# Kernel tuning notes

Hardware: AMD Instinct MI355X
Metric: run time of the kernel (lower is better)

The kernel has to match this reference:

```python
import jax, jax.numpy as jnp
import numpy as np

B, N_NODES, N_EDGES = 2, 40962, 327680
ND, ED, HD, L = 256, 64, 512, 16  # node_dim, edge_dim, hidden_dim, n_layers
LN_EPS = 1e-5


def _ln(x, g, b):
    m = jnp.mean(x, axis=-1, keepdims=True)
    v = jnp.var(x, axis=-1, keepdims=True)
    return (x - m) * jax.lax.rsqrt(v + LN_EPS) * g + b


def setup_inputs() -> dict:
    key = jax.random.key(0)
    ks = jax.random.split(key, 8)
    def w(k, shape, fan_in):
        return jax.random.normal(k, shape, jnp.float32) * (1.0 / np.sqrt(fan_in))
    node_features = jax.random.normal(ks[0], (B, N_NODES, ND), jnp.float32)
    edge_features = jax.random.normal(ks[1], (N_EDGES, ED), jnp.float32)
    edge_index = jax.random.randint(ks[2], (2, N_EDGES), 0, N_NODES, dtype=jnp.int32)
    ein, nin = ED + 2 * ND, ND + ED
    return {
        "node_features": node_features,
        "edge_features": edge_features,
        "We1": w(ks[3], (L, ein, HD), ein), "be1": jnp.zeros((L, HD), jnp.float32),
        "We2": w(ks[4], (L, HD, ED), HD),   "be2": jnp.zeros((L, ED), jnp.float32),
        "ge": jnp.ones((L, ED), jnp.float32), "ble": jnp.zeros((L, ED), jnp.float32),
        "Wn1": w(ks[5], (L, nin, HD), nin), "bn1": jnp.zeros((L, HD), jnp.float32),
        "Wn2": w(ks[6], (L, HD, ND), HD),   "bn2": jnp.zeros((L, ND), jnp.float32),
        "gn": jnp.ones((L, ND), jnp.float32), "bln": jnp.zeros((L, ND), jnp.float32),
        "edge_index": edge_index,
    }


def reference(node_features, edge_features, We1, be1, We2, be2, ge, ble,
              Wn1, bn1, Wn2, bn2, gn, bln, edge_index):
    src, dst = edge_index[0], edge_index[1]
    n = node_features.shape[-2]
    stacked = (We1, be1, We2, be2, ge, ble, Wn1, bn1, Wn2, bn2, gn, bln)

    def single(x0):  # x0: (N, ND) — original loops over batch; we vmap
        def layer(carry, p):
            x, e = carry
            we1, b1, we2, b2, g_e, b_e, wn1, nb1, wn2, nb2, g_n, b_n = p
            # edge update: gather endpoints, MLP, residual
            m = jnp.concatenate([e, x[src], x[dst]], axis=-1)   # (E, ED+2*ND)
            h = jax.nn.silu(m @ we1 + b1)                        # (E, HD)
            e = e + _ln(h @ we2 + b2, g_e, b_e)                  # (E, ED)
            # node update: scatter-sum messages to destinations, MLP, residual
            agg = jax.ops.segment_sum(e, dst, num_segments=n)    # (N, ED)
            h = jax.nn.silu(jnp.concatenate([x, agg], axis=-1) @ wn1 + nb1)
            x = x + _ln(h @ wn2 + nb2, g_n, b_n)                 # (N, ND)
            return (x, e), None
        (x, _e), _ = jax.lax.scan(layer, (x0, edge_features), stacked)
        return x

    return jax.vmap(single)(node_features)
```

## Files before the change

kernel.cpp:

```cpp
#include <hip/hip_runtime.h>
#include <hip/hip_bf16.h>

#define N_NODES 40962
#define N_EDGES 327680
#define NDIM 256
#define EDIM 64
#define HDIM 512
#define NLAYERS 16

using bf16_t = __bf16;
using bf16x4 = __bf16 __attribute__((ext_vector_type(4)));
using bf16x8 = __bf16 __attribute__((ext_vector_type(8)));
using f32x4  = float __attribute__((ext_vector_type(4)));

__device__ __forceinline__ void cvt_store4(bf16_t* p, float4 v) {
    bf16x4 t;
    t[0] = (bf16_t)v.x; t[1] = (bf16_t)v.y; t[2] = (bf16_t)v.z; t[3] = (bf16_t)v.w;
    *(bf16x4*)p = t;
}

__device__ __forceinline__ int clamp_idx(int v) {
    return v < 0 ? 0 : (v >= N_NODES ? N_NODES - 1 : v);
}

__global__ void repack_w(const float* __restrict__ src, bf16_t* __restrict__ dst,
                         int K, int N, int tilesPer) {
    int idx = blockIdx.x * 256 + threadIdx.x;
    int lane = idx & 63;
    int t = idx >> 6;
    int l = t / tilesPer;
    int tile = t % tilesPer;
    if (l >= NLAYERS) return;
    int ntN = N >> 4;
    int k0 = (tile / ntN) << 5;
    int n0 = (tile % ntN) << 4;
    int k = k0 + (lane >> 4) * 8;
    int n = n0 + (lane & 15);
    const float* s = src + (size_t)l * K * N + (size_t)k * N + n;
    bf16x8 v;
#pragma unroll
    for (int j = 0; j < 8; ++j) v[j] = (bf16_t)s[(size_t)j * N];
    *(bf16x8*)(dst + (size_t)idx * 8) = v;
}

__global__ void init_e2(const float* __restrict__ ef, bf16_t* __restrict__ es, int n8) {
    const size_t per = (size_t)N_EDGES * EDIM;
    for (int i = blockIdx.x * 256 + threadIdx.x; i < n8; i += gridDim.x * 256) {
        float4 a = *(const float4*)(ef + (size_t)i * 8);
        float4 b = *(const float4*)(ef + (size_t)i * 8 + 4);
        bf16x8 v;
        v[0] = (bf16_t)a.x; v[1] = (bf16_t)a.y; v[2] = (bf16_t)a.z; v[3] = (bf16_t)a.w;
        v[4] = (bf16_t)b.x; v[5] = (bf16_t)b.y; v[6] = (bf16_t)b.z; v[7] = (bf16_t)b.w;
        *(bf16x8*)(es + (size_t)i * 8) = v;
        *(bf16x8*)(es + per + (size_t)i * 8) = v;
    }
}

__global__ void zero_f32(float* __restrict__ p, int n4) {
    float4 z; z.x = z.y = z.z = z.w = 0.f;
    for (int i = blockIdx.x * 256 + threadIdx.x; i < n4; i += gridDim.x * 256)
        *(float4*)(p + (size_t)i * 4) = z;
}

__global__ __launch_bounds__(512, 4)
void edge_kernel(const float* __restrict__ xs, bf16_t* __restrict__ es,
                 float* __restrict__ agg, const int* __restrict__ eidx,
                 const bf16_t* __restrict__ w1p, const float* __restrict__ b1,
                 const bf16_t* __restrict__ w2p, const float* __restrict__ b2,
                 const float* __restrict__ gw, const float* __restrict__ bw) {
    __shared__ bf16_t smem[64 * 584];
    __shared__ int sSrc[64], sDst[64];
    float* red = (float*)(smem + 64 * 520);

    const int b   = blockIdx.y;
    const int e0  = blockIdx.x * 64;
    const int tid = threadIdx.x;

    const float* xb = xs + (size_t)b * N_NODES * NDIM;
    bf16_t* eb = es + (size_t)b * N_EDGES * EDIM;
    float* ab = agg + (size_t)b * N_NODES * EDIM;

    if (tid < 64) {
        sSrc[tid] = clamp_idx(eidx[e0 + tid]);
        sDst[tid] = clamp_idx(eidx[N_EDGES + e0 + tid]);
    }
    __syncthreads();

    {
        int r = tid >> 3, c = (tid & 7) << 3;
        *(bf16x8*)&smem[r * 584 + c] = *(const bf16x8*)(eb + (size_t)(e0 + r) * EDIM + c);
    }
#pragma unroll
    for (int k = 0; k < 8; ++k) {
        int i = tid + k * 512;
        int r = i >> 6, f = (i & 63) << 2;
        float4 v = *(const float4*)(xb + (size_t)sSrc[r] * NDIM + f);
        cvt_store4(&smem[r * 584 + 64 + f], v);
    }
#pragma unroll
    for (int k = 0; k < 8; ++k) {
        int i = tid + k * 512;
        int r = i >> 6, f = (i & 63) << 2;
        float4 v = *(const float4*)(xb + (size_t)sDst[r] * NDIM + f);
        cvt_store4(&smem[r * 584 + 320 + f], v);
    }
    __syncthreads();

    const int wv = tid >> 6, lane = tid & 63;
    const int m16 = lane & 15, quad = lane >> 4;

    float bias1[4];
#pragma unroll
    for (int nt = 0; nt < 4; ++nt) bias1[nt] = b1[wv * 64 + nt * 16 + m16];

    f32x4 acc1[4][4];
#pragma unroll
    for (int mt = 0; mt < 4; ++mt)
#pragma unroll
        for (int nt = 0; nt < 4; ++nt) acc1[mt][nt] = (f32x4){0.f, 0.f, 0.f, 0.f};

    const bf16x8* W1 = (const bf16x8*)w1p;
#pragma unroll 2
    for (int kc = 0; kc < 18; ++kc) {
        bf16x8 af[4];
#pragma unroll
        for (int mt = 0; mt < 4; ++mt)
            af[mt] = *(const bf16x8*)&smem[(mt * 16 + m16) * 584 + kc * 32 + quad * 8];
        bf16x8 bfr[4];
#pragma unroll
        for (int nt = 0; nt < 4; ++nt)
            bfr[nt] = W1[(size_t)(kc * 32 + wv * 4 + nt) * 64 + lane];
#pragma unroll
        for (int mt = 0; mt < 4; ++mt)
#pragma unroll
            for (int nt = 0; nt < 4; ++nt)
                acc1[mt][nt] = __builtin_amdgcn_mfma_f32_16x16x32_bf16(af[mt], bfr[nt], acc1[mt][nt], 0, 0, 0);
    }
    __syncthreads();

#pragma unroll
    for (int mt = 0; mt < 4; ++mt)
#pragma unroll
        for (int nt = 0; nt < 4; ++nt)
#pragma unroll
            for (int r = 0; r < 4; ++r) {
                int row = mt * 16 + quad * 4 + r;
                int col = wv * 64 + nt * 16 + m16;
                float v = acc1[mt][nt][r] + bias1[nt];
                v = v / (1.f + __expf(-v));
                smem[row * 520 + col] = (bf16_t)v;
            }
    __syncthreads();

    const int strip = wv >> 1, nh = wv & 1;
    f32x4 acc2[2];
#pragma unroll
    for (int nt = 0; nt < 2; ++nt) acc2[nt] = (f32x4){0.f, 0.f, 0.f, 0.f};
    const bf16x8* W2 = (const bf16x8*)w2p;
#pragma unroll 2
    for (int kc = 0; kc < 16; ++kc) {
        bf16x8 a2 = *(const bf16x8*)&smem[(strip * 16 + m16) * 520 + kc * 32 + quad * 8];
#pragma unroll
        for (int nt = 0; nt < 2; ++nt) {
            bf16x8 b2f = W2[(size_t)(kc * 4 + nh * 2 + nt) * 64 + lane];
            acc2[nt] = __builtin_amdgcn_mfma_f32_16x16x32_bf16(a2, b2f, acc2[nt], 0, 0, 0);
        }
    }

    float bias2[2], g2[2], bl2[2];
#pragma unroll
    for (int nt = 0; nt < 2; ++nt) {
        int c = nh * 32 + nt * 16 + m16;
        bias2[nt] = b2[c];
        g2[nt]    = gw[c];
        bl2[nt]   = bw[c];
    }
    float v[4][2];
#pragma unroll
    for (int r = 0; r < 4; ++r) {
        float s1 = 0.f, s2 = 0.f;
#pragma unroll
        for (int nt = 0; nt < 2; ++nt) {
            v[r][nt] = acc2[nt][r] + bias2[nt];
            s1 += v[r][nt]; s2 += v[r][nt] * v[r][nt];
        }
#pragma unroll
        for (int off = 1; off < 16; off <<= 1) {
            s1 += __shfl_xor(s1, off);
            s2 += __shfl_xor(s2, off);
        }
        if (m16 == 0) {
            int row = strip * 16 + quad * 4 + r;
            red[row * 4 + nh * 2 + 0] = s1;
            red[row * 4 + nh * 2 + 1] = s2;
        }
    }
    __syncthreads();

#pragma unroll
    for (int r = 0; r < 4; ++r) {
        int row = strip * 16 + quad * 4 + r;
        float s1 = red[row * 4 + 0] + red[row * 4 + 2];
        float s2 = red[row * 4 + 1] + red[row * 4 + 3];
        float mean = s1 * (1.f / 64.f);
        float var  = s2 * (1.f / 64.f) - mean * mean;
        float rstd = rsqrtf(fmaxf(var, 0.f) + 1e-5f);
        int eid = e0 + row;
        int d = sDst[row];
        bf16_t* ebr = eb + (size_t)eid * EDIM;
#pragma unroll
        for (int nt = 0; nt < 2; ++nt) {
            int c = nh * 32 + nt * 16 + m16;
            float ln = (v[r][nt] - mean) * rstd * g2[nt] + bl2[nt];
            float en = (float)ebr[c] + ln;
            ebr[c] = (bf16_t)en;
            atomicAdd(&ab[(size_t)d * EDIM + c], en);
        }
    }
}

__global__ __launch_bounds__(512, 4)
void node_kernel(float* __restrict__ xs, const float* __restrict__ agg,
                 const bf16_t* __restrict__ w1p, const float* __restrict__ b1,
                 const bf16_t* __restrict__ w2p, const float* __restrict__ b2,
                 const float* __restrict__ gw, const float* __restrict__ bw) {
    __shared__ bf16_t smem[64 * 528];
    float* red = (float*)(smem + 64 * 520);

    const int b   = blockIdx.y;
    const int n0  = blockIdx.x * 64;
    const int tid = threadIdx.x;

    float* xb = xs + (size_t)b * N_NODES * NDIM;
    const float* ab = agg + (size_t)b * N_NODES * EDIM;

    float4 z4; z4.x = z4.y = z4.z = z4.w = 0.f;
#pragma unroll
    for (int k = 0; k < 8; ++k) {
        int i = tid + k * 512;
        int r = i >> 6, f = (i & 63) << 2;
        int node = n0 + r;
        float4 v = (node < N_NODES) ? *(const float4*)(xb + (size_t)node * NDIM + f) : z4;
        cvt_store4(&smem[r * 328 + f], v);
    }
#pragma unroll
    for (int k = 0; k < 2; ++k) {
        int i = tid + k * 512;
        int r = i >> 4, f = (i & 15) << 2;
        int node = n0 + r;
        float4 v = (node < N_NODES) ? *(const float4*)(ab + (size_t)node * EDIM + f) : z4;
        cvt_store4(&smem[r * 328 + 256 + f], v);
    }
    __syncthreads();

    const int wv = tid >> 6, lane = tid & 63;
    const int m16 = lane & 15, quad = lane >> 4;

    float bias1[4];
#pragma unroll
    for (int nt = 0; nt < 4; ++nt) bias1[nt] = b1[wv * 64 + nt * 16 + m16];

    f32x4 acc1[4][4];
#pragma unroll
    for (int mt = 0; mt < 4; ++mt)
#pragma unroll
        for (int nt = 0; nt < 4; ++nt) acc1[mt][nt] = (f32x4){0.f, 0.f, 0.f, 0.f};

    const bf16x8* W1 = (const bf16x8*)w1p;
#pragma unroll 2
    for (int kc = 0; kc < 10; ++kc) {
        bf16x8 af[4];
#pragma unroll
        for (int mt = 0; mt < 4; ++mt)
            af[mt] = *(const bf16x8*)&smem[(mt * 16 + m16) * 328 + kc * 32 + quad * 8];
        bf16x8 bfr[4];
#pragma unroll
        for (int nt = 0; nt < 4; ++nt)
            bfr[nt] = W1[(size_t)(kc * 32 + wv * 4 + nt) * 64 + lane];
#pragma unroll
        for (int mt = 0; mt < 4; ++mt)
#pragma unroll
            for (int nt = 0; nt < 4; ++nt)
                acc1[mt][nt] = __builtin_amdgcn_mfma_f32_16x16x32_bf16(af[mt], bfr[nt], acc1[mt][nt], 0, 0, 0);
    }
    __syncthreads();

#pragma unroll
    for (int mt = 0; mt < 4; ++mt)
#pragma unroll
        for (int nt = 0; nt < 4; ++nt)
#pragma unroll
            for (int r = 0; r < 4; ++r) {
                int row = mt * 16 + quad * 4 + r;
                int col = wv * 64 + nt * 16 + m16;
                float v = acc1[mt][nt][r] + bias1[nt];
                v = v / (1.f + __expf(-v));
                smem[row * 520 + col] = (bf16_t)v;
            }
    __syncthreads();

    const int strip = wv >> 1, nh = wv & 1;
    f32x4 acc2[8];
#pragma unroll
    for (int nt = 0; nt < 8; ++nt) acc2[nt] = (f32x4){0.f, 0.f, 0.f, 0.f};
    const bf16x8* W2 = (const bf16x8*)w2p;
#pragma unroll 2
    for (int kc = 0; kc < 16; ++kc) {
        bf16x8 a2 = *(const bf16x8*)&smem[(strip * 16 + m16) * 520 + kc * 32 + quad * 8];
#pragma unroll
        for (int nt = 0; nt < 8; ++nt) {
            bf16x8 b2f = W2[(size_t)(kc * 16 + nh * 8 + nt) * 64 + lane];
            acc2[nt] = __builtin_amdgcn_mfma_f32_16x16x32_bf16(a2, b2f, acc2[nt], 0, 0, 0);
        }
    }

    float bias2[8], g8[8], bl8[8];
#pragma unroll
    for (int nt = 0; nt < 8; ++nt) {
        int c = nh * 128 + nt * 16 + m16;
        bias2[nt] = b2[c];
        g8[nt]    = gw[c];
        bl8[nt]   = bw[c];
    }
    float v[4][8];
#pragma unroll
    for (int r = 0; r < 4; ++r) {
        float s1 = 0.f, s2 = 0.f;
#pragma unroll
        for (int nt = 0; nt < 8; ++nt) {
            v[r][nt] = acc2[nt][r] + bias2[nt];
            s1 += v[r][nt]; s2 += v[r][nt] * v[r][nt];
        }
#pragma unroll
        for (int off = 1; off < 16; off <<= 1) {
            s1 += __shfl_xor(s1, off);
            s2 += __shfl_xor(s2, off);
        }
        if (m16 == 0) {
            int row = strip * 16 + quad * 4 + r;
            red[row * 4 + nh * 2 + 0] = s1;
            red[row * 4 + nh * 2 + 1] = s2;
        }
    }
    __syncthreads();

#pragma unroll
    for (int r = 0; r < 4; ++r) {
        int row = strip * 16 + quad * 4 + r;
        int node = n0 + row;
        if (node >= N_NODES) continue;
        float s1 = red[row * 4 + 0] + red[row * 4 + 2];
        float s2 = red[row * 4 + 1] + red[row * 4 + 3];
        float mean = s1 * (1.f / 256.f);
        float var  = s2 * (1.f / 256.f) - mean * mean;
        float rstd = rsqrtf(fmaxf(var, 0.f) + 1e-5f);
#pragma unroll
        for (int nt = 0; nt < 8; ++nt) {
            int c = nh * 128 + nt * 16 + m16;
            float ln = (v[r][nt] - mean) * rstd * g8[nt] + bl8[nt];
            xb[(size_t)node * NDIM + c] += ln;
        }
    }
}

extern "C" void kernel_launch(void* const* d_in, const int* in_sizes, int n_in,
                              void* d_out, int out_size, void* d_ws, size_t ws_size,
                              hipStream_t stream) {
    const float* nf   = (const float*)d_in[0];
    const float* ef   = (const float*)d_in[1];
    const float* We1  = (const float*)d_in[2];
    const float* be1  = (const float*)d_in[3];
    const float* We2  = (const float*)d_in[4];
    const float* be2  = (const float*)d_in[5];
    const float* ge   = (const float*)d_in[6];
    const float* ble  = (const float*)d_in[7];
    const float* Wn1  = (const float*)d_in[8];
    const float* bn1  = (const float*)d_in[9];
    const float* Wn2  = (const float*)d_in[10];
    const float* bn2  = (const float*)d_in[11];
    const float* gn   = (const float*)d_in[12];
    const float* bln  = (const float*)d_in[13];
    const int* eidx   = (const int*)d_in[14];

    float* xs = (float*)d_out;

    char* p = (char*)d_ws;
    bf16_t* es = (bf16_t*)p; p += (size_t)2 * N_EDGES * EDIM * 2;
    float*  ag = (float*)p;  p += (size_t)2 * N_NODES * EDIM * 4;
    bf16_t* w1ep = (bf16_t*)p; p += (size_t)NLAYERS * 576 * 512 * 2;
    bf16_t* w2ep = (bf16_t*)p; p += (size_t)NLAYERS * 512 * 64 * 2;
    bf16_t* w1np = (bf16_t*)p; p += (size_t)NLAYERS * 320 * 512 * 2;
    bf16_t* w2np = (bf16_t*)p; p += (size_t)NLAYERS * 512 * 256 * 2;

    repack_w<<<2304, 256, 0, stream>>>(We1, w1ep, 576, 512, 576);
    repack_w<<<256,  256, 0, stream>>>(We2, w2ep, 512, 64,  64);
    repack_w<<<1280, 256, 0, stream>>>(Wn1, w1np, 320, 512, 320);
    repack_w<<<1024, 256, 0, stream>>>(Wn2, w2np, 512, 256, 256);

    hipMemcpyAsync(xs, nf, (size_t)out_size * 4, hipMemcpyDeviceToDevice, stream);
    init_e2<<<2048, 256, 0, stream>>>(ef, es, N_EDGES * EDIM / 8);

    for (int l = 0; l < NLAYERS; ++l) {
        zero_f32<<<2048, 256, 0, stream>>>(ag, 2 * N_NODES * EDIM / 4);
        edge_kernel<<<dim3(N_EDGES / 64, 2), 512, 0, stream>>>(
            xs, es, ag, eidx,
            w1ep + (size_t)l * 576 * 512, be1 + l * 512,
            w2ep + (size_t)l * 512 * 64,  be2 + l * 64,
            ge + l * 64, ble + l * 64);
        node_kernel<<<dim3((N_NODES + 63) / 64, 2), 512, 0, stream>>>(
            xs, ag,
            w1np + (size_t)l * 320 * 512, bn1 + l * 512,
            w2np + (size_t)l * 512 * 256, bn2 + l * 256,
            gn + l * 256, bln + l * 256);
    }
}
```

Baseline: 13.29 ms.

## Replace atomic scatter with CSR gather aggregation and bf16 node mirror

Builds a destination-sorted CSR index once per call (histogram, scan, fill), and the node kernel now sums incoming edge features by gathering through it instead of the edge kernel doing fp32 atomicAdds into a zeroed buffer. It also keeps a bf16 copy of node features, updated in the node kernel, so the edge kernel gathers half as many bytes. Edge features are staged in shared memory and written back with vector stores. The cost is a serial single-block scan, per-node irregular gather loops with load imbalance, and aggregation summed from bf16-rounded edge values.

New measurement: 12.49 ms. 6.0% less time.

```diff
diff --git a/kernel.cpp b/kernel.cpp
--- a/kernel.cpp
+++ b/kernel.cpp
@@ -13,14 +13,15 @@
 using bf16x8 = __bf16 __attribute__((ext_vector_type(8)));
 using f32x4  = float __attribute__((ext_vector_type(4)));
 
-__device__ __forceinline__ void cvt_store4(bf16_t* p, float4 v) {
-    bf16x4 t;
-    t[0] = (bf16_t)v.x; t[1] = (bf16_t)v.y; t[2] = (bf16_t)v.z; t[3] = (bf16_t)v.w;
-    *(bf16x4*)p = t;
-}
-
 __device__ __forceinline__ int clamp_idx(int v) {
     return v < 0 ? 0 : (v >= N_NODES ? N_NODES - 1 : v);
+}
+
+__device__ __forceinline__ bf16x8 zero8() {
+    bf16x8 z;
+#pragma unroll
+    for (int j = 0; j < 8; ++j) z[j] = (bf16_t)0.f;
+    return z;
 }
 
 __global__ void repack_w(const float* __restrict__ src, bf16_t* __restrict__ dst,
@@ -56,15 +57,66 @@
     }
 }
 
+__global__ void f32_to_bf16(const float* __restrict__ src, bf16_t* __restrict__ dst, int n8) {
+    for (int i = blockIdx.x * 256 + threadIdx.x; i < n8; i += gridDim.x * 256) {
+        float4 a = *(const float4*)(src + (size_t)i * 8);
+        float4 b = *(const float4*)(src + (size_t)i * 8 + 4);
+        bf16x8 v;
+        v[0] = (bf16_t)a.x; v[1] = (bf16_t)a.y; v[2] = (bf16_t)a.z; v[3] = (bf16_t)a.w;
+        v[4] = (bf16_t)b.x; v[5] = (bf16_t)b.y; v[6] = (bf16_t)b.z; v[7] = (bf16_t)b.w;
+        *(bf16x8*)(dst + (size_t)i * 8) = v;
+    }
+}
+
 __global__ void zero_f32(float* __restrict__ p, int n4) {
     float4 z; z.x = z.y = z.z = z.w = 0.f;
     for (int i = blockIdx.x * 256 + threadIdx.x; i < n4; i += gridDim.x * 256)
         *(float4*)(p + (size_t)i * 4) = z;
 }
 
+__global__ void hist_k(const int* __restrict__ eidx, int* __restrict__ deg) {
+    int e = blockIdx.x * 256 + threadIdx.x;
+    if (e < N_EDGES) atomicAdd(&deg[clamp_idx(eidx[N_EDGES + e])], 1);
+}
+
+__global__ void scan_k(const int* __restrict__ deg, int* __restrict__ off,
+                       int* __restrict__ cur) {
+    __shared__ int part[1024];
+    const int t = threadIdx.x;
+    const int C = (N_NODES + 1023) / 1024;
+    int lo = t * C, hi = min((t + 1) * C, N_NODES);
+    int s = 0;
+    for (int i = lo; i < hi; ++i) s += deg[i];
+    part[t] = s;
+    __syncthreads();
+    for (int d = 1; d < 1024; d <<= 1) {
+        int v = (t >= d) ? part[t - d] : 0;
+        __syncthreads();
+        part[t] += v;
+        __syncthreads();
+    }
+    int base = (t == 0) ? 0 : part[t - 1];
+    for (int i = lo; i < hi; ++i) {
+        off[i] = base;
+        cur[i] = base;
+        base += deg[i];
+    }
+    if (t == 1023) off[N_NODES] = part[1023];
+}
+
+__global__ void fill_k(const int* __restrict__ eidx, int* __restrict__ cur,
+                       int* __restrict__ csr) {
+    int e = blockIdx.x * 256 + threadIdx.x;
+    if (e < N_EDGES) {
+        int d = clamp_idx(eidx[N_EDGES + e]);
+        int pos = atomicAdd(&cur[d], 1);
+        csr[pos] = e;
+    }
+}
+
 __global__ __launch_bounds__(512, 4)
-void edge_kernel(const float* __restrict__ xs, bf16_t* __restrict__ es,
-                 float* __restrict__ agg, const int* __restrict__ eidx,
+void edge_kernel(const bf16_t* __restrict__ x16, bf16_t* __restrict__ es,
+                 const int* __restrict__ eidx,
                  const bf16_t* __restrict__ w1p, const float* __restrict__ b1,
                  const bf16_t* __restrict__ w2p, const float* __restrict__ b2,
                  const float* __restrict__ gw, const float* __restrict__ bw) {
@@ -76,9 +128,8 @@
     const int e0  = blockIdx.x * 64;
     const int tid = threadIdx.x;
 
-    const float* xb = xs + (size_t)b * N_NODES * NDIM;
+    const bf16_t* xb = x16 + (size_t)b * N_NODES * NDIM;
     bf16_t* eb = es + (size_t)b * N_EDGES * EDIM;
-    float* ab = agg + (size_t)b * N_NODES * EDIM;
 
     if (tid < 64) {
         sSrc[tid] = clamp_idx(eidx[e0 + tid]);
@@ -91,18 +142,16 @@
         *(bf16x8*)&smem[r * 584 + c] = *(const bf16x8*)(eb + (size_t)(e0 + r) * EDIM + c);
     }
 #pragma unroll
-    for (int k = 0; k < 8; ++k) {
+    for (int k = 0; k < 4; ++k) {
         int i = tid + k * 512;
-        int r = i >> 6, f = (i & 63) << 2;
-        float4 v = *(const float4*)(xb + (size_t)sSrc[r] * NDIM + f);
-        cvt_store4(&smem[r * 584 + 64 + f], v);
-    }
-#pragma unroll
-    for (int k = 0; k < 8; ++k) {
+        int r = i >> 5, c = (i & 31) << 3;
+        *(bf16x8*)&smem[r * 584 + 64 + c] = *(const bf16x8*)(xb + (size_t)sSrc[r] * NDIM + c);
+    }
+#pragma unroll
+    for (int k = 0; k < 4; ++k) {
         int i = tid + k * 512;
-        int r = i >> 6, f = (i & 63) << 2;
-        float4 v = *(const float4*)(xb + (size_t)sDst[r] * NDIM + f);
-        cvt_store4(&smem[r * 584 + 320 + f], v);
+        int r = i >> 5, c = (i & 31) << 3;
+        *(bf16x8*)&smem[r * 584 + 320 + c] = *(const bf16x8*)(xb + (size_t)sDst[r] * NDIM + c);
     }
     __syncthreads();
 
@@ -206,21 +255,26 @@
         float var  = s2 * (1.f / 64.f) - mean * mean;
         float rstd = rsqrtf(fmaxf(var, 0.f) + 1e-5f);
         int eid = e0 + row;
-        int d = sDst[row];
-        bf16_t* ebr = eb + (size_t)eid * EDIM;
+        const bf16_t* ebr = eb + (size_t)eid * EDIM;
 #pragma unroll
         for (int nt = 0; nt < 2; ++nt) {
             int c = nh * 32 + nt * 16 + m16;
             float ln = (v[r][nt] - mean) * rstd * g2[nt] + bl2[nt];
             float en = (float)ebr[c] + ln;
-            ebr[c] = (bf16_t)en;
-            atomicAdd(&ab[(size_t)d * EDIM + c], en);
-        }
+            smem[row * 64 + c] = (bf16_t)en;
+        }
+    }
+    __syncthreads();
+    {
+        int r = tid >> 3, c = (tid & 7) << 3;
+        *(bf16x8*)(eb + (size_t)(e0 + r) * EDIM + c) = *(bf16x8*)&smem[r * 64 + c];
     }
 }
 
 __global__ __launch_bounds__(512, 4)
-void node_kernel(float* __restrict__ xs, const float* __restrict__ agg,
+void node_kernel(float* __restrict__ xs, bf16_t* __restrict__ x16,
+                 const bf16_t* __restrict__ es,
+                 const int* __restrict__ off, const int* __restrict__ csr,
                  const bf16_t* __restrict__ w1p, const float* __restrict__ b1,
                  const bf16_t* __restrict__ w2p, const float* __restrict__ b2,
                  const float* __restrict__ gw, const float* __restrict__ bw) {
@@ -232,29 +286,36 @@
     const int tid = threadIdx.x;
 
     float* xb = xs + (size_t)b * N_NODES * NDIM;
-    const float* ab = agg + (size_t)b * N_NODES * EDIM;
-
-    float4 z4; z4.x = z4.y = z4.z = z4.w = 0.f;
-#pragma unroll
-    for (int k = 0; k < 8; ++k) {
-        int i = tid + k * 512;
-        int r = i >> 6, f = (i & 63) << 2;
-        int node = n0 + r;
-        float4 v = (node < N_NODES) ? *(const float4*)(xb + (size_t)node * NDIM + f) : z4;
-        cvt_store4(&smem[r * 328 + f], v);
-    }
-#pragma unroll
-    for (int k = 0; k < 2; ++k) {
-        int i = tid + k * 512;
-        int r = i >> 4, f = (i & 15) << 2;
-        int node = n0 + r;
-        float4 v = (node < N_NODES) ? *(const float4*)(ab + (size_t)node * EDIM + f) : z4;
-        cvt_store4(&smem[r * 328 + 256 + f], v);
-    }
-    __syncthreads();
+    bf16_t* xhb = x16 + (size_t)b * N_NODES * NDIM;
+    const bf16_t* eb = es + (size_t)b * N_EDGES * EDIM;
 
     const int wv = tid >> 6, lane = tid & 63;
     const int m16 = lane & 15, quad = lane >> 4;
+
+#pragma unroll
+    for (int k = 0; k < 4; ++k) {
+        int i = tid + k * 512;
+        int r = i >> 5, c = (i & 31) << 3;
+        int node = n0 + r;
+        bf16x8 v = (node < N_NODES) ? *(const bf16x8*)(xhb + (size_t)node * NDIM + c)
+                                    : zero8();
+        *(bf16x8*)&smem[r * 328 + c] = v;
+    }
+#pragma unroll 1
+    for (int rr = 0; rr < 8; ++rr) {
+        int row = wv * 8 + rr;
+        int node = n0 + row;
+        float acc = 0.f;
+        if (node < N_NODES) {
+            int js = off[node], je = off[node + 1];
+            for (int j = js; j < je; ++j) {
+                int eid = csr[j];
+                acc += (float)eb[(size_t)eid * EDIM + lane];
+            }
+        }
+        smem[row * 328 + 256 + lane] = (bf16_t)acc;
+    }
+    __syncthreads();
 
     float bias1[4];
 #pragma unroll
@@ -332,9 +393,9 @@
             s1 += v[r][nt]; s2 += v[r][nt] * v[r][nt];
         }
 #pragma unroll
-        for (int off = 1; off < 16; off <<= 1) {
-            s1 += __shfl_xor(s1, off);
-            s2 += __shfl_xor(s2, off);
+        for (int off2 = 1; off2 < 16; off2 <<= 1) {
+            s1 += __shfl_xor(s1, off2);
+            s2 += __shfl_xor(s2, off2);
         }
         if (m16 == 0) {
             int row = strip * 16 + quad * 4 + r;
@@ -358,7 +419,10 @@
         for (int nt = 0; nt < 8; ++nt) {
             int c = nh * 128 + nt * 16 + m16;
             float ln = (v[r][nt] - mean) * rstd * g8[nt] + bl8[nt];
-            xb[(size_t)node * NDIM + c] += ln;
+            float* px = &xb[(size_t)node * NDIM + c];
+            float nv = *px + ln;
+            *px = nv;
+            xhb[(size_t)node * NDIM + c] = (bf16_t)nv;
         }
     }
 }
@@ -385,12 +449,16 @@
     float* xs = (float*)d_out;
 
     char* p = (char*)d_ws;
-    bf16_t* es = (bf16_t*)p; p += (size_t)2 * N_EDGES * EDIM * 2;
-    float*  ag = (float*)p;  p += (size_t)2 * N_NODES * EDIM * 4;
+    bf16_t* es  = (bf16_t*)p; p += (size_t)2 * N_EDGES * EDIM * 2;
+    bf16_t* x16 = (bf16_t*)p; p += (size_t)2 * N_NODES * NDIM * 2;
     bf16_t* w1ep = (bf16_t*)p; p += (size_t)NLAYERS * 576 * 512 * 2;
     bf16_t* w2ep = (bf16_t*)p; p += (size_t)NLAYERS * 512 * 64 * 2;
     bf16_t* w1np = (bf16_t*)p; p += (size_t)NLAYERS * 320 * 512 * 2;
     bf16_t* w2np = (bf16_t*)p; p += (size_t)NLAYERS * 512 * 256 * 2;
+    int* deg = (int*)p; p += (size_t)40964 * 4;
+    int* off = (int*)p; p += (size_t)40964 * 4;
+    int* cur = (int*)p; p += (size_t)40964 * 4;
+    int* csr = (int*)p; p += (size_t)N_EDGES * 4;
 
     repack_w<<<2304, 256, 0, stream>>>(We1, w1ep, 576, 512, 576);
     repack_w<<<256,  256, 0, stream>>>(We2, w2ep, 512, 64,  64);
@@ -398,17 +466,22 @@
     repack_w<<<1024, 256, 0, stream>>>(Wn2, w2np, 512, 256, 256);
 
     hipMemcpyAsync(xs, nf, (size_t)out_size * 4, hipMemcpyDeviceToDevice, stream);
+    f32_to_bf16<<<2048, 256, 0, stream>>>(nf, x16, 2 * N_NODES * NDIM / 8);
     init_e2<<<2048, 256, 0, stream>>>(ef, es, N_EDGES * EDIM / 8);
 
+    zero_f32<<<64, 256, 0, stream>>>((float*)deg, 40964 / 4);
+    hist_k<<<N_EDGES / 256, 256, 0, stream>>>(eidx, deg);
+    scan_k<<<1, 1024, 0, stream>>>(deg, off, cur);
+    fill_k<<<N_EDGES / 256, 256, 0, stream>>>(eidx, cur, csr);
+
     for (int l = 0; l < NLAYERS; ++l) {
-        zero_f32<<<2048, 256, 0, stream>>>(ag, 2 * N_NODES * EDIM / 4);
         edge_kernel<<<dim3(N_EDGES / 64, 2), 512, 0, stream>>>(
-            xs, es, ag, eidx,
+            x16, es, eidx,
             w1ep + (size_t)l * 576 * 512, be1 + l * 512,
             w2ep + (size_t)l * 512 * 64,  be2 + l * 64,
             ge + l * 64, ble + l * 64);
         node_kernel<<<dim3((N_NODES + 63) / 64, 2), 512, 0, stream>>>(
-            xs, ag,
+            xs, x16, es, off, csr,
             w1np + (size_t)l * 320 * 512, bn1 + l * 512,
             w2np + (size_t)l * 512 * 256, bn2 + l * 256,
             gn + l * 256, bln + l * 256);
```
